# Kernel tuning notes

Hardware: AMD Instinct MI355X
Metric: run time of the kernel (lower is better)

## Reference

```python
import jax, jax.numpy as jnp
import numpy as np

OBS = 128; N_AGENT = 16; N_ACTION = 8; N_LAYER = 2; HID = 128
GE = 256; LE = 256; F1 = 512; F2 = 512


def _edges(batch_size, n):
    # all ordered pairs (i, j), i != j, within each sample; GCNConv adds self-loops
    i, j = np.meshgrid(np.arange(n), np.arange(n), indexing='ij')
    m = i != j
    src0, dst0 = i[m], j[m]                      # [n*(n-1)]
    off = (np.arange(batch_size) * n)[:, None]
    src = (src0[None, :] + off).reshape(-1)
    dst = (dst0[None, :] + off).reshape(-1)
    return jnp.asarray(src, jnp.int32), jnp.asarray(dst, jnp.int32)


def setup_inputs() -> dict:
    key = jax.random.key(0)
    ks = jax.random.split(key, 16)
    g = lambda k, shp, fan: jax.random.normal(k, shp, jnp.float32) / np.sqrt(fan)
    return {
        'obs_j': jax.random.normal(ks[0], (2048, N_AGENT, OBS), jnp.float32),
        'W_pre': g(ks[1], (OBS, HID), OBS), 'b_pre': jnp.zeros((HID,), jnp.float32),
        'W_gcn': g(ks[2], (N_LAYER, HID, HID), HID), 'b_gcn': jnp.zeros((N_LAYER, HID), jnp.float32),
        'W_post': g(ks[3], (HID, GE), HID), 'b_post': jnp.zeros((GE,), jnp.float32),
        'W_loc': g(ks[4], (OBS, LE), OBS), 'b_loc': jnp.zeros((LE,), jnp.float32),
        'W1': g(ks[5], (GE + LE, F1), GE + LE), 'b1': jnp.zeros((F1,), jnp.float32),
        'W2': g(ks[6], (F1, F2), F1), 'b2': jnp.zeros((F2,), jnp.float32),
        'W3': g(ks[7], (F2, N_ACTION), F2), 'b3': jnp.zeros((N_ACTION,), jnp.float32),
    }


def reference(obs_j, W_pre, b_pre, W_gcn, b_gcn, W_post, b_post,
              W_loc, b_loc, W1, b1, W2, b2, W3, b3):
    B, n, _ = obs_j.shape
    N = B * n
    obs = obs_j.reshape(N, OBS)
    x = jax.nn.relu(obs @ W_pre + b_pre)          # [N, HID]

    src, dst = _edges(B, n)
    # GCNConv with self-loops on a fully-connected graph: deg = n for every node,
    # edge norm = 1/sqrt(deg_i*deg_j) = 1/n for every (A+I) edge.
    inv_n = jnp.float32(1.0) / n
    for l in range(N_LAYER):
        h = x @ W_gcn[l]                          # lin (no bias inside propagate)
        agg = jax.ops.segment_sum(h[src], dst, num_segments=N)  # neighbor gather/scatter
        x = jax.nn.relu((agg + h) * inv_n + b_gcn[l])            # + self-loop msg, bias

    g = x.reshape(B, n, HID).mean(axis=1)         # global_mean_pool over each graph
    g = jax.nn.relu(g @ W_post + b_post)          # [B, GE]
    loc = jax.nn.relu(obs @ W_loc + b_loc)        # [B*n, LE]
    gi = jnp.repeat(g, n, axis=0)                 # repeat_interleave over agents
    z = jnp.concatenate([gi, loc], axis=1)
    z = jax.nn.relu(z @ W1 + b1)
    z = jax.nn.relu(z @ W2 + b2)
    q = z @ W3 + b3
    return q.reshape(B, n, N_ACTION)
```

## Files before the change

kernel.cpp:

```cpp
#include <hip/hip_runtime.h>
#include <hip/hip_bf16.h>
#include <stdint.h>

typedef __bf16 bf16;
typedef __bf16 bf16x4 __attribute__((ext_vector_type(4)));
typedef __bf16 bf16x8 __attribute__((ext_vector_type(8)));
typedef float f32x4 __attribute__((ext_vector_type(4)));

#define MFMA(a, b, c) __builtin_amdgcn_mfma_f32_16x16x32_bf16(a, b, c, 0, 0, 0)
#define GL(p) ((const __attribute__((address_space(1))) void*)(p))
#define SH(p) ((__attribute__((address_space(3))) void*)(p))

__device__ inline void tp(const float* W, bf16* WT, int id, int shiftK, int N) {
  int K = 1 << shiftK;
  int n = id >> shiftK;
  int k = id & (K - 1);
  WT[id] = (bf16)W[(size_t)k * N + n];
}

__global__ __launch_bounds__(256) void prep_all(
    const float* __restrict__ W1, const float* __restrict__ W2,
    bf16* __restrict__ W1T, bf16* __restrict__ W2T,
    const float* __restrict__ Wpre, const float* __restrict__ Wloc,
    const float* __restrict__ Wgcn, const float* __restrict__ Wpost,
    bf16* __restrict__ WpreLocT, bf16* __restrict__ Wg0T, bf16* __restrict__ Wg1T,
    bf16* __restrict__ WpostT,
    const float* __restrict__ bpre, const float* __restrict__ bloc,
    float* __restrict__ biasPL, float* __restrict__ outq) {
  __shared__ bf16 tile[64 * 68];
  int blk = blockIdx.x;
  int tid = threadIdx.x;
  if (blk < 128) {
    const float* W = (blk < 64) ? W1 : W2;
    bf16* WT = (blk < 64) ? W1T : W2T;
    int t = blk & 63;
    int tk0 = (t >> 3) * 64, tn0 = (t & 7) * 64;
#pragma unroll
    for (int p = 0; p < 4; p++) {
      int kr = p * 16 + (tid >> 4), nc = (tid & 15) * 4;
      float4 f = *(const float4*)(W + (size_t)(tk0 + kr) * 512 + tn0 + nc);
      bf16x4 v; v[0] = (bf16)f.x; v[1] = (bf16)f.y; v[2] = (bf16)f.z; v[3] = (bf16)f.w;
      *(bf16x4*)&tile[kr * 68 + nc] = v;
    }
    __syncthreads();
#pragma unroll
    for (int p = 0; p < 4; p++) {
      int nr = p * 16 + (tid >> 4), kc = (tid & 15) * 4;
      bf16x4 v;
#pragma unroll
      for (int i = 0; i < 4; i++) v[i] = tile[(kc + i) * 68 + nr];
      *(bf16x4*)(WT + (size_t)(tn0 + nr) * 512 + tk0 + kc) = v;
    }
    return;
  }
  blk -= 128;
  if (blk < 448) {
    int id = blk * 256 + tid;
    if (id < 16384) { tp(Wpre, WpreLocT, id, 7, 128); return; } id -= 16384;
    if (id < 32768) { tp(Wloc, WpreLocT + 16384, id, 7, 256); return; } id -= 32768;
    if (id < 16384) { tp(Wgcn, Wg0T, id, 7, 128); return; } id -= 16384;
    if (id < 16384) { tp(Wgcn + 16384, Wg1T, id, 7, 128); return; } id -= 16384;
    tp(Wpost, WpostT, id, 7, 256);
    return;
  }
  blk -= 448;
  if (blk == 0) {
    if (tid < 128) biasPL[tid] = bpre[tid];
    biasPL[128 + tid] = bloc[tid];
    return;
  }
  blk -= 1;
  float4 z = {0.f, 0.f, 0.f, 0.f};
#pragma unroll
  for (int i = 0; i < 4; i++)
    ((float4*)outq)[(size_t)blk * 1024 + i * 256 + tid] = z;
}

__global__ __launch_bounds__(256, 4) void k1c(
    const float* __restrict__ obs, const bf16* __restrict__ WpreLocT,
    const float* __restrict__ biasPL,
    const bf16* __restrict__ Wg0T, const bf16* __restrict__ Wg1T,
    const bf16* __restrict__ WpostT, const float* __restrict__ b_gcn,
    const float* __restrict__ b_post,
    bf16* __restrict__ loc, bf16* __restrict__ g) {
  __shared__ bf16 smem[16384];
  bf16* As = smem;
  bf16* Bs = smem + 8192;

  const int tid = threadIdx.x;
  const int id = blockIdx.x;
  const int s = id >> 3;
  const int n_idx = s % 3;
  const int m0 = ((id & 7) + 8 * (s / 3)) * 128;
  const int n0 = n_idx * 128;

  f32x4 acc[4][4] = {};
  const int lane = tid & 63, wave = tid >> 6;
  const int wm = (wave >> 1) * 64, wn = (wave & 1) * 64;
  const int lm = lane & 15, quad = lane >> 4;

  for (int k0 = 0; k0 < 128; k0 += 64) {
#pragma unroll
    for (int it = 0; it < 4; it++) {
      int idx = it * 256 + tid;
      int row = idx >> 3;
      int c = idx & 7;
      int cv8 = c ^ (row & 7);
      int kk = k0 + cv8 * 8;
      const float* src = obs + (size_t)(m0 + row) * 128 + kk;
      float4 f0 = *(const float4*)src;
      float4 f1 = *(const float4*)(src + 4);
      bf16x8 v;
      v[0] = (bf16)f0.x; v[1] = (bf16)f0.y; v[2] = (bf16)f0.z; v[3] = (bf16)f0.w;
      v[4] = (bf16)f1.x; v[5] = (bf16)f1.y; v[6] = (bf16)f1.z; v[7] = (bf16)f1.w;
      *(bf16x8*)&As[row * 64 + c * 8] = v;
      const bf16* gb = WpreLocT + (size_t)(n0 + row) * 128 + kk;
      __builtin_amdgcn_global_load_lds(GL(gb), SH(&Bs[(idx & ~63) * 8]), 16, 0, 0);
    }
    __syncthreads();
#pragma unroll
    for (int ks = 0; ks < 2; ks++) {
      const int ua = quad + ks * 4;
      bf16x8 a[4], b[4];
#pragma unroll
      for (int i = 0; i < 4; i++) {
        int r = wm + lm + i * 16;
        a[i] = *(const bf16x8*)&As[r * 64 + ((ua ^ (r & 7)) * 8)];
      }
#pragma unroll
      for (int j = 0; j < 4; j++) {
        int r = wn + lm + j * 16;
        b[j] = *(const bf16x8*)&Bs[r * 64 + ((ua ^ (r & 7)) * 8)];
      }
#pragma unroll
      for (int i = 0; i < 4; i++)
#pragma unroll
        for (int j = 0; j < 4; j++)
          acc[i][j] = MFMA(a[i], b[j], acc[i][j]);
    }
    __syncthreads();
  }

  if (n_idx == 0) {
    bf16* xs = smem;
    bf16* x2 = smem + 2176;
#pragma unroll
    for (int i = 0; i < 4; i++) {
      int sl = (wave >> 1) * 4 + i;
#pragma unroll
      for (int j = 0; j < 4; j++) {
        int col = wn + j * 16 + lm;
        float bb = biasPL[col];
        float v = 0.f;
#pragma unroll
        for (int r = 0; r < 4; r++) v += fmaxf(acc[i][j][r] + bb, 0.f);
        v += __shfl_xor(v, 16);
        v += __shfl_xor(v, 32);
        if (quad == 0) xs[sl * 136 + col] = (bf16)(v * 0.0625f);
        else if (quad == 1) xs[(8 + sl) * 136 + col] = (bf16)0.f;
      }
    }
    __syncthreads();
    {
      f32x4 c2[2] = {};
#pragma unroll
      for (int ku = 0; ku < 4; ++ku) {
        bf16x8 a = *(const bf16x8*)&xs[lm * 136 + (ku * 4 + quad) * 8];
#pragma unroll
        for (int jn = 0; jn < 2; ++jn) {
          int col = (wave * 2 + jn) * 16 + lm;
          bf16x8 b = *(const bf16x8*)&Wg0T[(size_t)col * 128 + ku * 32 + quad * 8];
          c2[jn] = MFMA(a, b, c2[jn]);
        }
      }
      __syncthreads();
#pragma unroll
      for (int jn = 0; jn < 2; ++jn) {
        int col = (wave * 2 + jn) * 16 + lm;
        float bb = b_gcn[col];
#pragma unroll
        for (int r = 0; r < 4; ++r)
          x2[(quad * 4 + r) * 136 + col] = (bf16)fmaxf(c2[jn][r] + bb, 0.f);
      }
    }
    __syncthreads();
    {
      f32x4 c2[2] = {};
#pragma unroll
      for (int ku = 0; ku < 4; ++ku) {
        bf16x8 a = *(const bf16x8*)&x2[lm * 136 + (ku * 4 + quad) * 8];
#pragma unroll
        for (int jn = 0; jn < 2; ++jn) {
          int col = (wave * 2 + jn) * 16 + lm;
          bf16x8 b = *(const bf16x8*)&Wg1T[(size_t)col * 128 + ku * 32 + quad * 8];
          c2[jn] = MFMA(a, b, c2[jn]);
        }
      }
      __syncthreads();
#pragma unroll
      for (int jn = 0; jn < 2; ++jn) {
        int col = (wave * 2 + jn) * 16 + lm;
        float bb = b_gcn[128 + col];
#pragma unroll
        for (int r = 0; r < 4; ++r)
          xs[(quad * 4 + r) * 136 + col] = (bf16)fmaxf(c2[jn][r] + bb, 0.f);
      }
    }
    __syncthreads();
    {
      f32x4 c3[4] = {};
#pragma unroll
      for (int ku = 0; ku < 4; ++ku) {
        bf16x8 a = *(const bf16x8*)&xs[lm * 136 + (ku * 4 + quad) * 8];
#pragma unroll
        for (int jn = 0; jn < 4; ++jn) {
          int col = (wave * 4 + jn) * 16 + lm;
          bf16x8 b = *(const bf16x8*)&WpostT[(size_t)col * 128 + ku * 32 + quad * 8];
          c3[jn] = MFMA(a, b, c3[jn]);
        }
      }
      int sample0 = m0 >> 4;
#pragma unroll
      for (int jn = 0; jn < 4; ++jn) {
        int col = (wave * 4 + jn) * 16 + lm;
        float bb = b_post[col];
#pragma unroll
        for (int r = 0; r < 4; ++r) {
          int row = quad * 4 + r;
          if (row < 8)
            g[(size_t)(sample0 + row) * 256 + col] = (bf16)fmaxf(c3[jn][r] + bb, 0.f);
        }
      }
    }
  } else {
#pragma unroll
    for (int i = 0; i < 4; i++)
#pragma unroll
      for (int j = 0; j < 4; j++) {
        int col = wn + j * 16 + lm;
        float bb = biasPL[n0 + col];
#pragma unroll
        for (int r = 0; r < 4; r++) {
          int row = wm + i * 16 + quad * 4 + r;
          smem[row * 128 + col] = (bf16)fmaxf(acc[i][j][r] + bb, 0.f);
        }
      }
    __syncthreads();
    const int coff = n0 - 128;
#pragma unroll
    for (int c = 0; c < 8; c++) {
      int ci = c * 256 + tid;
      int row = ci >> 4, col8 = (ci & 15) * 8;
      *(bf16x8*)&loc[(size_t)(m0 + row) * 256 + coff + col8] = *(const bf16x8*)&smem[row * 128 + col8];
    }
  }
}

template <int ASRC, bool QFUSE>
__global__ __launch_bounds__(256, 4) void gemm_k(
    const bf16* __restrict__ Ab, const bf16* __restrict__ Ag,
    const bf16* __restrict__ BT, const float* __restrict__ bias,
    bf16* __restrict__ C,
    const float* __restrict__ W3, const float* __restrict__ b3,
    float* __restrict__ outq) {
  __shared__ bf16 smem[16384];
  bf16* As = smem;
  bf16* Bs = smem + 8192;

  const int tid = threadIdx.x;
  const int id = blockIdx.x;
  const int s = id >> 3;
  const int n_idx = s & 3;
  const int m0 = ((id & 7) + 8 * (s >> 2)) * 128;
  const int n0 = n_idx * 128;

  f32x4 acc[4][4] = {};
  const int lane = tid & 63, wave = tid >> 6;
  const int wm = (wave >> 1) * 64, wn = (wave & 1) * 64;
  const int lm = lane & 15, quad = lane >> 4;

  for (int k0 = 0; k0 < 512; k0 += 64) {
#pragma unroll
    for (int it = 0; it < 4; it++) {
      int idx = it * 256 + tid;
      int row = idx >> 3;
      int c = idx & 7;
      int cv8 = c ^ (row & 7);
      int kk = k0 + cv8 * 8;
      const bf16* ga;
      if (ASRC == 2) {
        int r = m0 + row;
        ga = (k0 < 256) ? (Ag + (size_t)(r >> 4) * 256 + kk)
                        : (Ab + (size_t)r * 256 + (kk - 256));
      } else {
        ga = Ab + (size_t)(m0 + row) * 512 + kk;
      }
      __builtin_amdgcn_global_load_lds(GL(ga), SH(&As[(idx & ~63) * 8]), 16, 0, 0);
      const bf16* gb = BT + (size_t)(n0 + row) * 512 + kk;
      __builtin_amdgcn_global_load_lds(GL(gb), SH(&Bs[(idx & ~63) * 8]), 16, 0, 0);
    }
    __syncthreads();
#pragma unroll
    for (int ks = 0; ks < 2; ks++) {
      const int ua = quad + ks * 4;
      bf16x8 a[4], b[4];
#pragma unroll
      for (int i = 0; i < 4; i++) {
        int r = wm + lm + i * 16;
        a[i] = *(const bf16x8*)&As[r * 64 + ((ua ^ (r & 7)) * 8)];
      }
#pragma unroll
      for (int j = 0; j < 4; j++) {
        int r = wn + lm + j * 16;
        b[j] = *(const bf16x8*)&Bs[r * 64 + ((ua ^ (r & 7)) * 8)];
      }
#pragma unroll
      for (int i = 0; i < 4; i++)
#pragma unroll
        for (int j = 0; j < 4; j++)
          acc[i][j] = MFMA(a[i], b[j], acc[i][j]);
    }
    __syncthreads();
  }

  if (QFUSE) {
#pragma unroll
    for (int i = 0; i < 4; i++)
#pragma unroll
      for (int j = 0; j < 4; j++) {
        int col = wn + j * 16 + lm;
        float bb = bias[n0 + col];
#pragma unroll
        for (int r = 0; r < 4; r++) {
          int row = wm + i * 16 + quad * 4 + r;
          smem[row * 128 + col] = (bf16)fmaxf(acc[i][j][r] + bb, 0.f);
        }
      }
    __syncthreads();
    int n = lane & 7;
    int kg = lane >> 3;
    float w3r[16];
#pragma unroll
    for (int i = 0; i < 16; i++) w3r[i] = W3[(size_t)(n0 + kg * 16 + i) * 8 + n];
    float bn = (n_idx == 0) ? b3[n] : 0.f;
    int rbase = wave * 32;
    for (int rr = 0; rr < 32; rr++) {
      const bf16* zr = &smem[(rbase + rr) * 128 + kg * 16];
      bf16x8 z0 = *(const bf16x8*)zr;
      bf16x8 z1v = *(const bf16x8*)(zr + 8);
      float v = 0.f;
#pragma unroll
      for (int i = 0; i < 8; i++) v += (float)z0[i] * w3r[i];
#pragma unroll
      for (int i = 0; i < 8; i++) v += (float)z1v[i] * w3r[8 + i];
      v += __shfl_down(v, 32);
      v += __shfl_down(v, 16);
      v += __shfl_down(v, 8);
      if (lane < 8) atomicAdd(&outq[(size_t)(m0 + rbase + rr) * 8 + n], v + bn);
    }
  } else {
#pragma unroll
    for (int i = 0; i < 4; i++)
#pragma unroll
      for (int j = 0; j < 4; j++) {
        int col = wn + j * 16 + lm;
        float bb = bias[n0 + col];
#pragma unroll
        for (int r = 0; r < 4; r++) {
          int row = wm + i * 16 + quad * 4 + r;
          smem[row * 128 + col] = (bf16)fmaxf(acc[i][j][r] + bb, 0.f);
        }
      }
    __syncthreads();
#pragma unroll
    for (int c = 0; c < 8; c++) {
      int ci = c * 256 + tid;
      int row = ci >> 4, col8 = (ci & 15) * 8;
      *(bf16x8*)&C[(size_t)(m0 + row) * 512 + n0 + col8] = *(const bf16x8*)&smem[row * 128 + col8];
    }
  }
}

extern "C" void kernel_launch(void* const* d_in, const int* in_sizes, int n_in,
                              void* d_out, int out_size, void* d_ws, size_t ws_size,
                              hipStream_t stream) {
  const float* obs    = (const float*)d_in[0];
  const float* W_pre  = (const float*)d_in[1];
  const float* b_pre  = (const float*)d_in[2];
  const float* W_gcn  = (const float*)d_in[3];
  const float* b_gcn  = (const float*)d_in[4];
  const float* W_post = (const float*)d_in[5];
  const float* b_post = (const float*)d_in[6];
  const float* W_loc  = (const float*)d_in[7];
  const float* b_loc  = (const float*)d_in[8];
  const float* W1     = (const float*)d_in[9];
  const float* b1     = (const float*)d_in[10];
  const float* W2     = (const float*)d_in[11];
  const float* b2     = (const float*)d_in[12];
  const float* W3     = (const float*)d_in[13];
  const float* b3     = (const float*)d_in[14];
  float* out = (float*)d_out;

  char* p = (char*)d_ws;
  auto alloc = [&](size_t bytes) { char* r = p; p += (bytes + 255) & ~(size_t)255; return r; };
  bf16* WpreLocT = (bf16*)alloc(384 * 128 * 2);
  float* biasPL  = (float*)alloc(384 * 4);
  bf16* Wg0T   = (bf16*)alloc(128 * 128 * 2);
  bf16* Wg1T   = (bf16*)alloc(128 * 128 * 2);
  bf16* WpostT = (bf16*)alloc(256 * 128 * 2);
  bf16* W1T    = (bf16*)alloc(512 * 512 * 2);
  bf16* W2T    = (bf16*)alloc(512 * 512 * 2);
  bf16* locB   = (bf16*)alloc((size_t)32768 * 256 * 2);
  bf16* gB     = (bf16*)alloc(2048 * 256 * 2);
  bf16* z1B    = (bf16*)alloc((size_t)32768 * 512 * 2);

  prep_all<<<641, 256, 0, stream>>>(W1, W2, W1T, W2T,
                                    W_pre, W_loc, W_gcn, W_post,
                                    WpreLocT, Wg0T, Wg1T, WpostT,
                                    b_pre, b_loc, biasPL, out);
  k1c<<<768, 256, 0, stream>>>(obs, WpreLocT, biasPL,
                               Wg0T, Wg1T, WpostT, b_gcn, b_post,
                               locB, gB);
  gemm_k<2, false><<<1024, 256, 0, stream>>>(locB, gB, W1T, b1, z1B,
                                             nullptr, nullptr, nullptr);
  gemm_k<0, true><<<1024, 256, 0, stream>>>(z1B, nullptr, W2T, b2, nullptr,
                                            W3, b3, out);
}
```

Before: 169.3 us.

## Pre-convert obs to bf16 and rebalance prep work across kernels

Adds a bf16 copy of obs, made in the prep kernel, so k1c can stream its A tiles into LDS with global_load_lds instead of loading fp32 and converting in registers. The W1/W2 transposes move into extra blocks of k1c, and zeroing the output moves into extra blocks of the first MLP GEMM, so that work overlaps with compute kernels. The cost is an extra 8 MB bf16 buffer written and read back, plus larger grids with branchy tail blocks.

```diff
diff --git a/kernel.cpp b/kernel.cpp
--- a/kernel.cpp
+++ b/kernel.cpp
@@ -18,42 +18,47 @@
   WT[id] = (bf16)W[(size_t)k * N + n];
 }
 
+__device__ inline void big_tp(const float* W, bf16* WT, int t, int tid, bf16* tile) {
+  int tk0 = (t >> 3) * 64, tn0 = (t & 7) * 64;
+#pragma unroll
+  for (int p = 0; p < 4; p++) {
+    int kr = p * 16 + (tid >> 4), nc = (tid & 15) * 4;
+    float4 f = *(const float4*)(W + (size_t)(tk0 + kr) * 512 + tn0 + nc);
+    bf16x4 v; v[0] = (bf16)f.x; v[1] = (bf16)f.y; v[2] = (bf16)f.z; v[3] = (bf16)f.w;
+    *(bf16x4*)&tile[kr * 68 + nc] = v;
+  }
+  __syncthreads();
+#pragma unroll
+  for (int p = 0; p < 4; p++) {
+    int nr = p * 16 + (tid >> 4), kc = (tid & 15) * 4;
+    bf16x4 v;
+#pragma unroll
+    for (int i = 0; i < 4; i++) v[i] = tile[(kc + i) * 68 + nr];
+    *(bf16x4*)(WT + (size_t)(tn0 + nr) * 512 + tk0 + kc) = v;
+  }
+}
+
 __global__ __launch_bounds__(256) void prep_all(
-    const float* __restrict__ W1, const float* __restrict__ W2,
-    bf16* __restrict__ W1T, bf16* __restrict__ W2T,
+    const float* __restrict__ obs, bf16* __restrict__ obs_bf,
     const float* __restrict__ Wpre, const float* __restrict__ Wloc,
     const float* __restrict__ Wgcn, const float* __restrict__ Wpost,
     bf16* __restrict__ WpreLocT, bf16* __restrict__ Wg0T, bf16* __restrict__ Wg1T,
     bf16* __restrict__ WpostT,
     const float* __restrict__ bpre, const float* __restrict__ bloc,
-    float* __restrict__ biasPL, float* __restrict__ outq) {
-  __shared__ bf16 tile[64 * 68];
+    float* __restrict__ biasPL) {
   int blk = blockIdx.x;
   int tid = threadIdx.x;
-  if (blk < 128) {
-    const float* W = (blk < 64) ? W1 : W2;
-    bf16* WT = (blk < 64) ? W1T : W2T;
-    int t = blk & 63;
-    int tk0 = (t >> 3) * 64, tn0 = (t & 7) * 64;
-#pragma unroll
-    for (int p = 0; p < 4; p++) {
-      int kr = p * 16 + (tid >> 4), nc = (tid & 15) * 4;
-      float4 f = *(const float4*)(W + (size_t)(tk0 + kr) * 512 + tn0 + nc);
-      bf16x4 v; v[0] = (bf16)f.x; v[1] = (bf16)f.y; v[2] = (bf16)f.z; v[3] = (bf16)f.w;
-      *(bf16x4*)&tile[kr * 68 + nc] = v;
-    }
-    __syncthreads();
-#pragma unroll
-    for (int p = 0; p < 4; p++) {
-      int nr = p * 16 + (tid >> 4), kc = (tid & 15) * 4;
-      bf16x4 v;
-#pragma unroll
-      for (int i = 0; i < 4; i++) v[i] = tile[(kc + i) * 68 + nr];
-      *(bf16x4*)(WT + (size_t)(tn0 + nr) * 512 + tk0 + kc) = v;
-    }
+  if (blk < 2048) {
+    int id = blk * 256 + tid;
+    const float4* s = (const float4*)(obs + (size_t)id * 8);
+    float4 f0 = s[0], f1 = s[1];
+    bf16x8 v;
+    v[0] = (bf16)f0.x; v[1] = (bf16)f0.y; v[2] = (bf16)f0.z; v[3] = (bf16)f0.w;
+    v[4] = (bf16)f1.x; v[5] = (bf16)f1.y; v[6] = (bf16)f1.z; v[7] = (bf16)f1.w;
+    *(bf16x8*)(obs_bf + (size_t)id * 8) = v;
     return;
   }
-  blk -= 128;
+  blk -= 2048;
   if (blk < 448) {
     int id = blk * 256 + tid;
     if (id < 16384) { tp(Wpre, WpreLocT, id, 7, 128); return; } id -= 16384;
@@ -63,32 +68,31 @@
     tp(Wpost, WpostT, id, 7, 256);
     return;
   }
-  blk -= 448;
-  if (blk == 0) {
-    if (tid < 128) biasPL[tid] = bpre[tid];
-    biasPL[128 + tid] = bloc[tid];
-    return;
-  }
-  blk -= 1;
-  float4 z = {0.f, 0.f, 0.f, 0.f};
-#pragma unroll
-  for (int i = 0; i < 4; i++)
-    ((float4*)outq)[(size_t)blk * 1024 + i * 256 + tid] = z;
+  if (tid < 128) biasPL[tid] = bpre[tid];
+  biasPL[128 + tid] = bloc[tid];
 }
 
 __global__ __launch_bounds__(256, 4) void k1c(
-    const float* __restrict__ obs, const bf16* __restrict__ WpreLocT,
+    const bf16* __restrict__ obs_bf, const bf16* __restrict__ WpreLocT,
     const float* __restrict__ biasPL,
     const bf16* __restrict__ Wg0T, const bf16* __restrict__ Wg1T,
     const bf16* __restrict__ WpostT, const float* __restrict__ b_gcn,
     const float* __restrict__ b_post,
-    bf16* __restrict__ loc, bf16* __restrict__ g) {
+    bf16* __restrict__ loc, bf16* __restrict__ g,
+    const float* __restrict__ W1, const float* __restrict__ W2,
+    bf16* __restrict__ W1T, bf16* __restrict__ W2T) {
   __shared__ bf16 smem[16384];
+  const int tid = threadIdx.x;
+  const int id = blockIdx.x;
+
+  if (id >= 768) {
+    int b = id - 768;
+    big_tp((b < 64) ? W1 : W2, (b < 64) ? W1T : W2T, b & 63, tid, smem);
+    return;
+  }
+
   bf16* As = smem;
   bf16* Bs = smem + 8192;
-
-  const int tid = threadIdx.x;
-  const int id = blockIdx.x;
   const int s = id >> 3;
   const int n_idx = s % 3;
   const int m0 = ((id & 7) + 8 * (s / 3)) * 128;
@@ -107,13 +111,8 @@
       int c = idx & 7;
       int cv8 = c ^ (row & 7);
       int kk = k0 + cv8 * 8;
-      const float* src = obs + (size_t)(m0 + row) * 128 + kk;
-      float4 f0 = *(const float4*)src;
-      float4 f1 = *(const float4*)(src + 4);
-      bf16x8 v;
-      v[0] = (bf16)f0.x; v[1] = (bf16)f0.y; v[2] = (bf16)f0.z; v[3] = (bf16)f0.w;
-      v[4] = (bf16)f1.x; v[5] = (bf16)f1.y; v[6] = (bf16)f1.z; v[7] = (bf16)f1.w;
-      *(bf16x8*)&As[row * 64 + c * 8] = v;
+      const bf16* ga = obs_bf + (size_t)(m0 + row) * 128 + kk;
+      __builtin_amdgcn_global_load_lds(GL(ga), SH(&As[(idx & ~63) * 8]), 16, 0, 0);
       const bf16* gb = WpreLocT + (size_t)(n0 + row) * 128 + kk;
       __builtin_amdgcn_global_load_lds(GL(gb), SH(&Bs[(idx & ~63) * 8]), 16, 0, 0);
     }
@@ -256,7 +255,7 @@
   }
 }
 
-template <int ASRC, bool QFUSE>
+template <int ASRC, bool QFUSE, bool ZTAIL>
 __global__ __launch_bounds__(256, 4) void gemm_k(
     const bf16* __restrict__ Ab, const bf16* __restrict__ Ag,
     const bf16* __restrict__ BT, const float* __restrict__ bias,
@@ -264,11 +263,20 @@
     const float* __restrict__ W3, const float* __restrict__ b3,
     float* __restrict__ outq) {
   __shared__ bf16 smem[16384];
+  const int tid = threadIdx.x;
+  const int id = blockIdx.x;
+
+  if (ZTAIL && id >= 1024) {
+    int b = id - 1024;
+    float4 z = {0.f, 0.f, 0.f, 0.f};
+#pragma unroll
+    for (int i = 0; i < 4; i++)
+      ((float4*)outq)[(size_t)b * 1024 + i * 256 + tid] = z;
+    return;
+  }
+
   bf16* As = smem;
   bf16* Bs = smem + 8192;
-
-  const int tid = threadIdx.x;
-  const int id = blockIdx.x;
   const int s = id >> 3;
   const int n_idx = s & 3;
   const int m0 = ((id & 7) + 8 * (s >> 2)) * 128;
@@ -410,19 +418,20 @@
   bf16* WpostT = (bf16*)alloc(256 * 128 * 2);
   bf16* W1T    = (bf16*)alloc(512 * 512 * 2);
   bf16* W2T    = (bf16*)alloc(512 * 512 * 2);
+  bf16* obs_bf = (bf16*)alloc((size_t)32768 * 128 * 2);
   bf16* locB   = (bf16*)alloc((size_t)32768 * 256 * 2);
   bf16* gB     = (bf16*)alloc(2048 * 256 * 2);
   bf16* z1B    = (bf16*)alloc((size_t)32768 * 512 * 2);
 
-  prep_all<<<641, 256, 0, stream>>>(W1, W2, W1T, W2T,
-                                    W_pre, W_loc, W_gcn, W_post,
-                                    WpreLocT, Wg0T, Wg1T, WpostT,
-                                    b_pre, b_loc, biasPL, out);
-  k1c<<<768, 256, 0, stream>>>(obs, WpreLocT, biasPL,
+  prep_all<<<2497, 256, 0, stream>>>(obs, obs_bf,
+                                     W_pre, W_loc, W_gcn, W_post,
+                                     WpreLocT, Wg0T, Wg1T, WpostT,
+                                     b_pre, b_loc, biasPL);
+  k1c<<<896, 256, 0, stream>>>(obs_bf, WpreLocT, biasPL,
                                Wg0T, Wg1T, WpostT, b_gcn, b_post,
-                               locB, gB);
-  gemm_k<2, false><<<1024, 256, 0, stream>>>(locB, gB, W1T, b1, z1B,
-                                             nullptr, nullptr, nullptr);
-  gemm_k<0, true><<<1024, 256, 0, stream>>>(z1B, nullptr, W2T, b2, nullptr,
-                                            W3, b3, out);
-}
+                               locB, gB, W1, W2, W1T, W2T);
+  gemm_k<2, false, true><<<1088, 256, 0, stream>>>(locB, gB, W1T, b1, z1B,
+                                                   nullptr, nullptr, out);
+  gemm_k<0, true, false><<<1024, 256, 0, stream>>>(z1B, nullptr, W2T, b2, nullptr,
+                                                   W3, b3, out);
+}
```

Measured after the change: 176.1 us. +4.0%, slower.

## Precompute per-sample global half of first MLP layer, halve K of W1 GEMM

Applied to the files above, without the earlier changes.

The global embedding g is identical for all 16 agents of a sample, so its product with the first half of W1 (plus b1) is now computed once per sample inside k1c and stored as fp32. The main W1 GEMM then only runs over the 256 local features, adding the per-sample partial sum in the epilogue. This removes the redundant half of the K loop for the first MLP layer. In exchange k1c does extra per-sample MFMA work and the epilogue gathers an fp32 row per sample.

```diff
diff --git a/kernel.cpp b/kernel.cpp
--- a/kernel.cpp
+++ b/kernel.cpp
@@ -82,7 +82,8 @@
     const bf16* __restrict__ Wg0T, const bf16* __restrict__ Wg1T,
     const bf16* __restrict__ WpostT, const float* __restrict__ b_gcn,
     const float* __restrict__ b_post,
-    bf16* __restrict__ loc, bf16* __restrict__ g) {
+    const bf16* __restrict__ W1T, const float* __restrict__ b1,
+    bf16* __restrict__ loc, float* __restrict__ h) {
   __shared__ bf16 smem[16384];
   bf16* As = smem;
   bf16* Bs = smem + 8192;
@@ -144,6 +145,7 @@
   if (n_idx == 0) {
     bf16* xs = smem;
     bf16* x2 = smem + 2176;
+    bf16* gS = smem + 4352;
 #pragma unroll
     for (int i = 0; i < 4; i++) {
       int sl = (wave >> 1) * 4 + i;
@@ -219,16 +221,38 @@
           c3[jn] = MFMA(a, b, c3[jn]);
         }
       }
-      int sample0 = m0 >> 4;
 #pragma unroll
       for (int jn = 0; jn < 4; ++jn) {
         int col = (wave * 4 + jn) * 16 + lm;
         float bb = b_post[col];
 #pragma unroll
+        for (int r = 0; r < 4; ++r)
+          gS[(quad * 4 + r) * 264 + col] = (bf16)fmaxf(c3[jn][r] + bb, 0.f);
+      }
+    }
+    __syncthreads();
+    {
+      f32x4 hacc[8] = {};
+#pragma unroll
+      for (int ku = 0; ku < 8; ++ku) {
+        bf16x8 a = *(const bf16x8*)&gS[lm * 264 + ku * 32 + quad * 8];
+#pragma unroll
+        for (int jn = 0; jn < 8; ++jn) {
+          int col = (wave * 8 + jn) * 16 + lm;
+          bf16x8 b = *(const bf16x8*)&W1T[(size_t)col * 512 + ku * 32 + quad * 8];
+          hacc[jn] = MFMA(a, b, hacc[jn]);
+        }
+      }
+      int sample0 = m0 >> 4;
+#pragma unroll
+      for (int jn = 0; jn < 8; ++jn) {
+        int col = (wave * 8 + jn) * 16 + lm;
+        float bb = b1[col];
+#pragma unroll
         for (int r = 0; r < 4; ++r) {
           int row = quad * 4 + r;
           if (row < 8)
-            g[(size_t)(sample0 + row) * 256 + col] = (bf16)fmaxf(c3[jn][r] + bb, 0.f);
+            h[(size_t)(sample0 + row) * 512 + col] = hacc[jn][r] + bb;
         }
       }
     }
@@ -256,10 +280,10 @@
   }
 }
 
-template <int ASRC, bool QFUSE>
+template <bool HREP>
 __global__ __launch_bounds__(256, 4) void gemm_k(
-    const bf16* __restrict__ Ab, const bf16* __restrict__ Ag,
-    const bf16* __restrict__ BT, const float* __restrict__ bias,
+    const bf16* __restrict__ Ab, const bf16* __restrict__ BT,
+    const float* __restrict__ bias, const float* __restrict__ hrep,
     bf16* __restrict__ C,
     const float* __restrict__ W3, const float* __restrict__ b3,
     float* __restrict__ outq) {
@@ -279,7 +303,8 @@
   const int wm = (wave >> 1) * 64, wn = (wave & 1) * 64;
   const int lm = lane & 15, quad = lane >> 4;
 
-  for (int k0 = 0; k0 < 512; k0 += 64) {
+  const int KTOT = HREP ? 256 : 512;
+  for (int k0 = 0; k0 < KTOT; k0 += 64) {
 #pragma unroll
     for (int it = 0; it < 4; it++) {
       int idx = it * 256 + tid;
@@ -287,16 +312,11 @@
       int c = idx & 7;
       int cv8 = c ^ (row & 7);
       int kk = k0 + cv8 * 8;
-      const bf16* ga;
-      if (ASRC == 2) {
-        int r = m0 + row;
-        ga = (k0 < 256) ? (Ag + (size_t)(r >> 4) * 256 + kk)
-                        : (Ab + (size_t)r * 256 + (kk - 256));
-      } else {
-        ga = Ab + (size_t)(m0 + row) * 512 + kk;
-      }
+      const bf16* ga = HREP ? (Ab + (size_t)(m0 + row) * 256 + kk)
+                            : (Ab + (size_t)(m0 + row) * 512 + kk);
       __builtin_amdgcn_global_load_lds(GL(ga), SH(&As[(idx & ~63) * 8]), 16, 0, 0);
-      const bf16* gb = BT + (size_t)(n0 + row) * 512 + kk;
+      const bf16* gb = HREP ? (BT + (size_t)(n0 + row) * 512 + 256 + kk)
+                            : (BT + (size_t)(n0 + row) * 512 + kk);
       __builtin_amdgcn_global_load_lds(GL(gb), SH(&Bs[(idx & ~63) * 8]), 16, 0, 0);
     }
     __syncthreads();
@@ -323,7 +343,29 @@
     __syncthreads();
   }
 
-  if (QFUSE) {
+  if (HREP) {
+#pragma unroll
+    for (int i = 0; i < 4; i++) {
+      int sample = (m0 + wm + i * 16) >> 4;
+#pragma unroll
+      for (int j = 0; j < 4; j++) {
+        int col = n0 + wn + j * 16 + lm;
+        float hv = hrep[(size_t)sample * 512 + col];
+#pragma unroll
+        for (int r = 0; r < 4; r++) {
+          int row = wm + i * 16 + quad * 4 + r;
+          smem[row * 128 + (col - n0)] = (bf16)fmaxf(acc[i][j][r] + hv, 0.f);
+        }
+      }
+    }
+    __syncthreads();
+#pragma unroll
+    for (int c = 0; c < 8; c++) {
+      int ci = c * 256 + tid;
+      int row = ci >> 4, col8 = (ci & 15) * 8;
+      *(bf16x8*)&C[(size_t)(m0 + row) * 512 + n0 + col8] = *(const bf16x8*)&smem[row * 128 + col8];
+    }
+  } else {
 #pragma unroll
     for (int i = 0; i < 4; i++)
 #pragma unroll
@@ -357,26 +399,6 @@
       v += __shfl_down(v, 16);
       v += __shfl_down(v, 8);
       if (lane < 8) atomicAdd(&outq[(size_t)(m0 + rbase + rr) * 8 + n], v + bn);
-    }
-  } else {
-#pragma unroll
-    for (int i = 0; i < 4; i++)
-#pragma unroll
-      for (int j = 0; j < 4; j++) {
-        int col = wn + j * 16 + lm;
-        float bb = bias[n0 + col];
-#pragma unroll
-        for (int r = 0; r < 4; r++) {
-          int row = wm + i * 16 + quad * 4 + r;
-          smem[row * 128 + col] = (bf16)fmaxf(acc[i][j][r] + bb, 0.f);
-        }
-      }
-    __syncthreads();
-#pragma unroll
-    for (int c = 0; c < 8; c++) {
-      int ci = c * 256 + tid;
-      int row = ci >> 4, col8 = (ci & 15) * 8;
-      *(bf16x8*)&C[(size_t)(m0 + row) * 512 + n0 + col8] = *(const bf16x8*)&smem[row * 128 + col8];
     }
   }
 }
@@ -411,7 +433,7 @@
   bf16* W1T    = (bf16*)alloc(512 * 512 * 2);
   bf16* W2T    = (bf16*)alloc(512 * 512 * 2);
   bf16* locB   = (bf16*)alloc((size_t)32768 * 256 * 2);
-  bf16* gB     = (bf16*)alloc(2048 * 256 * 2);
+  float* hB    = (float*)alloc((size_t)2048 * 512 * 4);
   bf16* z1B    = (bf16*)alloc((size_t)32768 * 512 * 2);
 
   prep_all<<<641, 256, 0, stream>>>(W1, W2, W1T, W2T,
@@ -420,9 +442,9 @@
                                     b_pre, b_loc, biasPL, out);
   k1c<<<768, 256, 0, stream>>>(obs, WpreLocT, biasPL,
                                Wg0T, Wg1T, WpostT, b_gcn, b_post,
-                               locB, gB);
-  gemm_k<2, false><<<1024, 256, 0, stream>>>(locB, gB, W1T, b1, z1B,
-                                             nullptr, nullptr, nullptr);
-  gemm_k<0, true><<<1024, 256, 0, stream>>>(z1B, nullptr, W2T, b2, nullptr,
-                                            W3, b3, out);
+                               W1T, b1, locB, hB);
+  gemm_k<true><<<1024, 256, 0, stream>>>(locB, W1T, nullptr, hB, z1B,
+                                         nullptr, nullptr, nullptr);
+  gemm_k<false><<<1024, 256, 0, stream>>>(z1B, W2T, b2, nullptr, nullptr,
+                                          W3, b3, out);
 }
```

Result: no change. 172.0 us (median of 2 runs) (+1.6%).
